# Kernel tuning notes

Hardware: AMD Instinct MI355X
Metric: run time of the kernel (lower is better)

The kernel has to match this reference:

```python
import jax, jax.numpy as jnp
import numpy as np

N = 50000          # nodes
E = 800000         # edges per graph view
D_IN = 256
D_HID = 128
N_CLS = 40
EPS = 1e-12


def agnn_conv(x, src, dst, beta):
    """DGL AGNNConv: cosine edge attention + edge softmax + weighted aggregation."""
    # L2-normalize node features (F.normalize, eps=1e-12)
    norm = jnp.sqrt(jnp.sum(x * x, axis=1, keepdims=True))
    hn = x / jnp.maximum(norm, EPS)                      # [N, D]
    # cosine similarity per edge, scaled by learned beta
    e = beta * jnp.sum(hn[src] * hn[dst], axis=1)        # [E]
    # segment (per-destination) stable softmax
    m = jax.ops.segment_max(e, dst, num_segments=N)      # [N]
    m = jnp.where(jnp.isfinite(m), m, 0.0)               # empty segments -> -inf
    ee = jnp.exp(e - m[dst])                             # [E]
    s = jax.ops.segment_sum(ee, dst, num_segments=N)     # [N]
    a = ee / jnp.maximum(s[dst], EPS)                    # [E]
    # weighted sparse aggregation of ORIGINAL (un-normalized) features
    return jax.ops.segment_sum(a[:, None] * x[src], dst, num_segments=N)


def setup_inputs() -> dict:
    key = jax.random.key(0)
    ks = jax.random.split(key, 10)
    return {
        "input_features": jax.random.normal(ks[0], (N, D_IN), dtype=jnp.float32),
        "src1": jax.random.randint(ks[1], (E,), 0, N, dtype=jnp.int32),
        "dst1": jax.random.randint(ks[2], (E,), 0, N, dtype=jnp.int32),
        "src2": jax.random.randint(ks[3], (E,), 0, N, dtype=jnp.int32),
        "dst2": jax.random.randint(ks[4], (E,), 0, N, dtype=jnp.int32),
        "order_attn": jax.random.uniform(ks[5], (2,), dtype=jnp.float32),
        "W1": jax.random.normal(ks[6], (D_IN, D_HID), dtype=jnp.float32) * (2.0 / np.sqrt(D_IN + D_HID)),
        "b1": jnp.zeros((D_HID,), dtype=jnp.float32),
        "W2": jax.random.normal(ks[7], (D_HID, N_CLS), dtype=jnp.float32) * (2.0 / np.sqrt(D_HID + N_CLS)),
        "b2": jnp.zeros((N_CLS,), dtype=jnp.float32),
        "beta1": jnp.ones((), dtype=jnp.float32),
        "beta2": jnp.ones((), dtype=jnp.float32),
    }


def reference(input_features, src1, dst1, src2, dst2, order_attn, W1, b1, W2, b2, beta1, beta2):
    # fc1 + relu
    x1 = jax.nn.relu(input_features @ W1 + b1)           # [N, D_HID]
    # layer1 over both graph views, combined by learned order_attn scalars
    x2 = order_attn[0] * agnn_conv(x1, src1, dst1, beta1) \
       + order_attn[1] * agnn_conv(x1, src2, dst2, beta1)
    # layer2 over both views
    x3 = order_attn[0] * agnn_conv(x2, src1, dst1, beta2) \
       + order_attn[1] * agnn_conv(x2, src2, dst2, beta2)
    # fc2 (original computes F.log_softmax but discards it; returns logits)
    return x3 @ W2 + b2                                   # [N, N_CLS]
```

## Files before the change

### kernel.cpp

```cpp
#include <hip/hip_runtime.h>
#include <hip/hip_fp16.h>
#include <math.h>

#define NNODES 50000
#define NEDGES 800000
#define DIN    256
#define DHID   128
#define NCLS   40

#define BW    128
#define NBK   391
#define CAP   6144
#define PPART 128
#define CHUNK 6250

typedef _Float16 h2v __attribute__((ext_vector_type(2)));
union HF8 { float4 f; __half2 h2[4]; h2v v[4]; };
union HF4 { float2 f; __half2 h2[2]; };

__global__ __launch_bounds__(256) void fc1_kernel(
    const float* __restrict__ X, const float* __restrict__ W1,
    const float* __restrict__ b1, __half* __restrict__ x1h,
    float* __restrict__ inv1)
{
  __shared__ float As[64][65];
  __shared__ float Bs[64][132];
  const int tid   = threadIdx.x;
  const int node0 = blockIdx.x * 64;
  const int tx    = tid & 15;
  const int ty    = tid >> 4;

  const int ml   = tid >> 2;
  const int kq   = tid & 3;
  const int mrow = (node0 + ml < NNODES) ? node0 + ml : NNODES - 1;

  float acc[4][8];
#pragma unroll
  for (int i = 0; i < 4; ++i)
#pragma unroll
    for (int j = 0; j < 8; ++j) acc[i][j] = 0.f;

  for (int kt = 0; kt < 4; ++kt) {
    const int k0 = kt * 64;
#pragma unroll
    for (int q = 0; q < 4; ++q) {
      const int kk = kq * 16 + q * 4;
      const float4 v = *(const float4*)(X + (size_t)mrow * DIN + k0 + kk);
      As[kk + 0][ml] = v.x; As[kk + 1][ml] = v.y;
      As[kk + 2][ml] = v.z; As[kk + 3][ml] = v.w;
    }
#pragma unroll
    for (int q = 0; q < 8; ++q) {
      const int flat = q * 1024 + tid * 4;
      const int kk = flat >> 7, nn = flat & 127;
      *(float4*)&Bs[kk][nn] = *(const float4*)(W1 + (size_t)(k0 + kk) * DHID + nn);
    }
    __syncthreads();

#pragma unroll 4
    for (int k = 0; k < 64; ++k) {
      const float4 a  = *(const float4*)&As[k][ty * 4];
      const float4 b0 = *(const float4*)&Bs[k][tx * 4];
      const float4 b1v= *(const float4*)&Bs[k][64 + tx * 4];
      const float av[4] = {a.x, a.y, a.z, a.w};
      const float bv[8] = {b0.x, b0.y, b0.z, b0.w, b1v.x, b1v.y, b1v.z, b1v.w};
#pragma unroll
      for (int i = 0; i < 4; ++i)
#pragma unroll
        for (int j = 0; j < 8; ++j) acc[i][j] += av[i] * bv[j];
    }
    __syncthreads();
  }

  const float4 bb0 = *(const float4*)(b1 + tx * 4);
  const float4 bb1 = *(const float4*)(b1 + 64 + tx * 4);
  const float bias[8] = {bb0.x, bb0.y, bb0.z, bb0.w, bb1.x, bb1.y, bb1.z, bb1.w};

#pragma unroll
  for (int i = 0; i < 4; ++i) {
    const int row = node0 + ty * 4 + i;
    float v[8];
    float q = 0.f;
#pragma unroll
    for (int j = 0; j < 8; ++j) {
      float t = acc[i][j] + bias[j];
      t = t > 0.f ? t : 0.f;
      v[j] = t;
      q += t * t;
    }
    q += __shfl_xor(q, 1);
    q += __shfl_xor(q, 2);
    q += __shfl_xor(q, 4);
    q += __shfl_xor(q, 8);
    if (row < NNODES) {
      HF4 o0, o1;
      o0.h2[0] = __floats2half2_rn(v[0], v[1]);
      o0.h2[1] = __floats2half2_rn(v[2], v[3]);
      o1.h2[0] = __floats2half2_rn(v[4], v[5]);
      o1.h2[1] = __floats2half2_rn(v[6], v[7]);
      *(float2*)(x1h + (size_t)row * DHID + tx * 4)      = o0.f;
      *(float2*)(x1h + (size_t)row * DHID + 64 + tx * 4) = o1.f;
      if (tx == 0) inv1[row] = 1.0f / fmaxf(sqrtf(q), 1e-12f);
    }
  }
}

__global__ __launch_bounds__(320) void fc2_kernel(
    const float* __restrict__ x3, const float* __restrict__ W2,
    const float* __restrict__ b2, float* __restrict__ out)
{
  __shared__ float Xs[8][DHID];
  const int tid   = threadIdx.x;
  const int node0 = blockIdx.x * 8;
  for (int idx = tid; idx < 8 * DHID; idx += 320)
    Xs[idx >> 7][idx & 127] = x3[(size_t)node0 * DHID + idx];
  __syncthreads();

  const int ns = tid / NCLS;
  const int c  = tid - ns * NCLS;
  float acc = b2[c];
#pragma unroll 8
  for (int k = 0; k < DHID; ++k) acc += Xs[ns][k] * W2[k * NCLS + c];
  out[(size_t)(node0 + ns) * NCLS + c] = acc;
}

__global__ __launch_bounds__(256) void hist_part_kernel(
    const int* __restrict__ dst1, const int* __restrict__ dst2,
    int* __restrict__ H)
{
  const int bid = blockIdx.x;
  const int v   = bid >= PPART;
  const int p   = v ? bid - PPART : bid;
  const int* __restrict__ dst = v ? dst2 : dst1;

  __shared__ int hist[NBK];
  for (int i = threadIdx.x; i < NBK; i += 256) hist[i] = 0;
  __syncthreads();
  const int beg = p * CHUNK;
  const int end = (beg + CHUNK < NEDGES) ? beg + CHUNK : NEDGES;
  for (int j = beg + threadIdx.x; j < end; j += 256)
    atomicAdd(&hist[dst[j] >> 7], 1);
  __syncthreads();
  for (int i = threadIdx.x; i < NBK; i += 256)
    H[(v * NBK + i) * PPART + p] = hist[i];
}

__global__ __launch_bounds__(128) void scan_bucket_kernel(
    int* __restrict__ H, int* __restrict__ btot)
{
  const int b   = blockIdx.x;
  const int tid = threadIdx.x;
  __shared__ int sm[PPART];
  const int v = H[b * PPART + tid];
  sm[tid] = v;
  __syncthreads();
  for (int off = 1; off < PPART; off <<= 1) {
    int t = (tid >= off) ? sm[tid - off] : 0;
    __syncthreads();
    sm[tid] += t;
    __syncthreads();
  }
  H[b * PPART + tid] = sm[tid] - v;
  if (tid == PPART - 1) btot[b] = sm[tid];
}

__global__ __launch_bounds__(1024) void scan_btot_kernel(
    const int* __restrict__ btot, int* __restrict__ boffG)
{
  __shared__ int sm[1024];
  const int tid = threadIdx.x;
  const int v = (tid < 2 * NBK) ? btot[tid] : 0;
  sm[tid] = v;
  __syncthreads();
  for (int off = 1; off < 1024; off <<= 1) {
    int t = (tid >= off) ? sm[tid - off] : 0;
    __syncthreads();
    sm[tid] += t;
    __syncthreads();
  }
  if (tid < 2 * NBK) boffG[tid] = sm[tid] - v;
  if (tid == 0) boffG[2 * NBK] = 2 * NEDGES;
}

__global__ __launch_bounds__(256) void scatter_part_kernel(
    const int* __restrict__ src1, const int* __restrict__ dst1,
    const int* __restrict__ src2, const int* __restrict__ dst2,
    const int* __restrict__ H, const int* __restrict__ boffG,
    int2* __restrict__ st)
{
  const int bid = blockIdx.x;
  const int v   = bid >= PPART;
  const int p   = v ? bid - PPART : bid;
  const int* __restrict__ src = v ? src2 : src1;
  const int* __restrict__ dst = v ? dst2 : dst1;

  __shared__ int lcur[NBK];
  for (int i = threadIdx.x; i < NBK; i += 256)
    lcur[i] = boffG[v * NBK + i] + H[(v * NBK + i) * PPART + p];
  __syncthreads();
  const int beg = p * CHUNK;
  const int end = (beg + CHUNK < NEDGES) ? beg + CHUNK : NEDGES;
  for (int j = beg + threadIdx.x; j < end; j += 256) {
    const int s = src[j], d = dst[j];
    const int k = atomicAdd(&lcur[d >> 7], 1);
    st[k] = make_int2(s, d);
  }
}

__global__ __launch_bounds__(256) void build_buckets_kernel(
    const int2* __restrict__ st, const int* __restrict__ boffG,
    int* __restrict__ rp1, int* __restrict__ rp2,
    int* __restrict__ col1, int* __restrict__ col2)
{
  const int bid = blockIdx.x;
  const int v   = bid >= NBK;
  const int b   = v ? bid - NBK : bid;
  int* __restrict__ rp  = v ? rp2 : rp1;
  int* __restrict__ col = v ? col2 : col1;
  const int tid = threadIdx.x;

  const int off0G  = boffG[bid];
  const int cnt    = boffG[bid + 1] - off0G;
  const int off0   = off0G - v * NEDGES;
  const int base_d = b * BW;
  const int nd     = (NNODES - base_d < BW) ? (NNODES - base_d) : BW;

  __shared__ int deg[BW];
  __shared__ int loff[BW + 1];
  __shared__ int cur[BW];
  __shared__ int lcol[CAP];

  if (tid < BW) deg[tid] = 0;
  __syncthreads();
  for (int j = tid; j < cnt; j += 256)
    atomicAdd(&deg[st[off0G + j].y - base_d], 1);
  __syncthreads();

  if (tid == 0) loff[0] = 0;
  if (tid < BW) loff[tid + 1] = deg[tid];
  __syncthreads();
  for (int off = 1; off < BW; off <<= 1) {
    int t = (tid < BW && tid + 1 >= off) ? loff[tid + 1 - off] : 0;
    __syncthreads();
    if (tid < BW && tid + 1 >= off) loff[tid + 1] += t;
    __syncthreads();
  }
  if (tid < nd) rp[base_d + tid] = off0 + loff[tid];
  if (tid == 0 && b == NBK - 1) rp[NNODES] = NEDGES;
  if (tid < BW) cur[tid] = loff[tid];
  __syncthreads();

  if (cnt <= CAP) {
    for (int j = tid; j < cnt; j += 256) {
      const int2 pr = st[off0G + j];
      const int k = atomicAdd(&cur[pr.y - base_d], 1);
      lcol[k] = pr.x;
    }
    __syncthreads();
    if (tid < nd) {
      const int s0 = loff[tid], s1 = s0 + deg[tid];
      for (int a = s0 + 1; a < s1; ++a) {
        const int key = lcol[a];
        int c = a - 1;
        while (c >= s0 && lcol[c] > key) { lcol[c + 1] = lcol[c]; --c; }
        lcol[c + 1] = key;
      }
    }
    __syncthreads();
    for (int j = tid; j < cnt; j += 256) col[off0 + j] = lcol[j];
  } else {
    for (int j = tid; j < cnt; j += 256) {
      const int2 pr = st[off0G + j];
      const int k = atomicAdd(&cur[pr.y - base_d], 1);
      col[off0 + k] = pr.x;
    }
    __syncthreads();
    if (tid < nd) {
      const int s0 = off0 + loff[tid], s1 = s0 + deg[tid];
      for (int a = s0 + 1; a < s1; ++a) {
        const int key = col[a];
        int c = a - 1;
        while (c >= s0 && col[c] > key) { col[c + 1] = col[c]; --c; }
        col[c + 1] = key;
      }
    }
  }
}

__global__ __launch_bounds__(256) void agnn_layer_kernel(
    const __half* __restrict__ xh, const float* __restrict__ inv,
    const int* __restrict__ rp1, const int* __restrict__ col1,
    const int* __restrict__ rp2, const int* __restrict__ col2,
    const float* __restrict__ beta_p, const float* __restrict__ order_attn,
    __half* __restrict__ yh_out, float* __restrict__ inv_out,
    float* __restrict__ y32_out, int n)
{
  const int wid  = (blockIdx.x * blockDim.x + threadIdx.x) >> 6;
  if (wid >= n) return;
  const int lane = threadIdx.x & 63;
  const int grp  = lane >> 4;
  const int sub  = lane & 15;

  const float beta = beta_p[0];
  const float bi   = beta * inv[wid];

  HF8 ud; ud.f = *(const float4*)(xh + (size_t)wid * DHID + sub * 8);

  const int beg1 = rp1[wid], end1 = rp1[wid + 1];
  const int beg2 = rp2[wid], end2 = rp2[wid + 1];

  float s1 = 0.f, s2 = 0.f;
  float y1[8], y2[8];
#pragma unroll
  for (int k = 0; k < 8; ++k) { y1[k] = 0.f; y2[k] = 0.f; }

  int j1 = beg1 + grp, j2 = beg2 + grp;
  int sa1 = col1[j1 < end1 ? j1 : 0];
  int sa2 = col2[j2 < end2 ? j2 : 0];

  while (j1 < end1 || j2 < end2) {
    const bool p1 = j1 < end1;
    const bool p2 = j2 < end2;
    const int  c1 = sa1, c2 = sa2;

    const float isa1 = inv[c1];
    const float isa2 = inv[c2];
    HF8 u1; u1.f = *(const float4*)(xh + (size_t)c1 * DHID + sub * 8);
    HF8 u2; u2.f = *(const float4*)(xh + (size_t)c2 * DHID + sub * 8);

    const int nj1 = j1 + 4, nj2 = j2 + 4;
    sa1 = col1[nj1 < end1 ? nj1 : 0];
    sa2 = col2[nj2 < end2 ? nj2 : 0];

    float d1 = 0.f, d2 = 0.f;
#pragma unroll
    for (int i = 0; i < 4; ++i) {
      d1 = __builtin_amdgcn_fdot2(u1.v[i], ud.v[i], d1, false);
      d2 = __builtin_amdgcn_fdot2(u2.v[i], ud.v[i], d2, false);
    }
#pragma unroll
    for (int off = 1; off <= 8; off <<= 1) {
      d1 += __shfl_xor(d1, off);
      d2 += __shfl_xor(d2, off);
    }

    const float w1 = p1 ? __expf(bi * isa1 * d1) : 0.f;
    const float w2 = p2 ? __expf(bi * isa2 * d2) : 0.f;
    s1 += w1; s2 += w2;
#pragma unroll
    for (int i = 0; i < 4; ++i) {
      y1[2 * i + 0] = fmaf(w1, (float)u1.v[i][0], y1[2 * i + 0]);
      y1[2 * i + 1] = fmaf(w1, (float)u1.v[i][1], y1[2 * i + 1]);
      y2[2 * i + 0] = fmaf(w2, (float)u2.v[i][0], y2[2 * i + 0]);
      y2[2 * i + 1] = fmaf(w2, (float)u2.v[i][1], y2[2 * i + 1]);
    }

    j1 = nj1; j2 = nj2;
  }

  s1 += __shfl_xor(s1, 16); s1 += __shfl_xor(s1, 32);
  s2 += __shfl_xor(s2, 16); s2 += __shfl_xor(s2, 32);
#pragma unroll
  for (int k = 0; k < 8; ++k) {
    y1[k] += __shfl_xor(y1[k], 16); y1[k] += __shfl_xor(y1[k], 32);
    y2[k] += __shfl_xor(y2[k], 16); y2[k] += __shfl_xor(y2[k], 32);
  }

  const float r1 = (end1 > beg1) ? order_attn[0] / fmaxf(s1, 1e-12f) : 0.f;
  const float r2 = (end2 > beg2) ? order_attn[1] / fmaxf(s2, 1e-12f) : 0.f;
  float acc[8];
#pragma unroll
  for (int k = 0; k < 8; ++k) acc[k] = r1 * y1[k] + r2 * y2[k];

  if (inv_out) {
    float ss = 0.f;
#pragma unroll
    for (int k = 0; k < 8; ++k) ss += acc[k] * acc[k];
    ss += __shfl_xor(ss, 1);
    ss += __shfl_xor(ss, 2);
    ss += __shfl_xor(ss, 4);
    ss += __shfl_xor(ss, 8);
    if (lane == 0) inv_out[wid] = 1.0f / fmaxf(sqrtf(ss), 1e-12f);
  }

  if (grp == 0) {
    if (yh_out) {
      HF8 o;
      o.h2[0] = __floats2half2_rn(acc[0], acc[1]);
      o.h2[1] = __floats2half2_rn(acc[2], acc[3]);
      o.h2[2] = __floats2half2_rn(acc[4], acc[5]);
      o.h2[3] = __floats2half2_rn(acc[6], acc[7]);
      *(float4*)(yh_out + (size_t)wid * DHID + sub * 8) = o.f;
    }
    if (y32_out) {
      float* yp = y32_out + (size_t)wid * DHID + sub * 8;
      *(float4*)(yp)     = make_float4(acc[0], acc[1], acc[2], acc[3]);
      *(float4*)(yp + 4) = make_float4(acc[4], acc[5], acc[6], acc[7]);
    }
  }
}

extern "C" void kernel_launch(void* const* d_in, const int* in_sizes, int n_in,
                              void* d_out, int out_size, void* d_ws, size_t ws_size,
                              hipStream_t stream)
{
  const float* X          = (const float*)d_in[0];
  const int*   src1       = (const int*)d_in[1];
  const int*   dst1       = (const int*)d_in[2];
  const int*   src2       = (const int*)d_in[3];
  const int*   dst2       = (const int*)d_in[4];
  const float* order_attn = (const float*)d_in[5];
  const float* W1         = (const float*)d_in[6];
  const float* b1         = (const float*)d_in[7];
  const float* W2         = (const float*)d_in[8];
  const float* b2         = (const float*)d_in[9];
  const float* beta1      = (const float*)d_in[10];
  const float* beta2      = (const float*)d_in[11];
  float*       out        = (float*)d_out;

  char*  ws  = (char*)d_ws;
  size_t off = 0;
  auto alloc = [&](size_t bytes) -> void* {
    void* p = ws + off;
    off += (bytes + 255) & ~size_t(255);
    return p;
  };
  __half* x1h  = (__half*)alloc((size_t)NNODES * DHID * 2);
  __half* x2h  = (__half*)alloc((size_t)NNODES * DHID * 2);
  float*  x3   = (float*)alloc((size_t)NNODES * DHID * 4);
  float*  inv1 = (float*)alloc((size_t)NNODES * 4);
  float*  inv2 = (float*)alloc((size_t)NNODES * 4);
  int*    rp1  = (int*)alloc((size_t)(NNODES + 1) * 4);
  int*    rp2  = (int*)alloc((size_t)(NNODES + 1) * 4);
  int*    col1 = (int*)alloc((size_t)NEDGES * 4);
  int*    col2 = (int*)alloc((size_t)NEDGES * 4);
  int*    H    = (int*)alloc((size_t)2 * NBK * PPART * 4);
  int*    btot = (int*)alloc((size_t)2 * NBK * 4);
  int*    boffG= (int*)alloc((size_t)(2 * NBK + 1) * 4);
  int2*   st   = (int2*)x3;

  const int WB = (NNODES + 3) / 4;

  hist_part_kernel<<<2 * PPART, 256, 0, stream>>>(dst1, dst2, H);
  scan_bucket_kernel<<<2 * NBK, 128, 0, stream>>>(H, btot);
  scan_btot_kernel<<<1, 1024, 0, stream>>>(btot, boffG);
  scatter_part_kernel<<<2 * PPART, 256, 0, stream>>>(src1, dst1, src2, dst2,
                                                     H, boffG, st);
  build_buckets_kernel<<<2 * NBK, 256, 0, stream>>>(st, boffG, rp1, rp2, col1, col2);

  fc1_kernel<<<(NNODES + 63) / 64, 256, 0, stream>>>(X, W1, b1, x1h, inv1);

  agnn_layer_kernel<<<WB, 256, 0, stream>>>(x1h, inv1, rp1, col1, rp2, col2,
                                            beta1, order_attn,
                                            x2h, inv2, nullptr, NNODES);
  agnn_layer_kernel<<<WB, 256, 0, stream>>>(x2h, inv2, rp1, col1, rp2, col2,
                                            beta2, order_attn,
                                            nullptr, nullptr, x3, NNODES);

  fc2_kernel<<<NNODES / 8, 320, 0, stream>>>(x3, W2, b2, out);
}
```

Before: 300.4 us.

## Use DPP row reductions, fp16 final layer output, padded column arrays, 32-bit indexing

Replaces the shuffle-based 16-lane reductions with DPP row operations. It stores the second AGNN layer output in fp16 instead of fp32, which halves the write and the fc2 read. The column index arrays are padded with zeros so the prefetch loads need no bounds select, and 32-bit unsigned address arithmetic replaces 64-bit. The sort staging buffer now gets its own allocation because x3 shrank, and the fp16 x3 adds some precision loss before fc2.

```diff
diff --git a/kernel.cpp b/kernel.cpp
--- a/kernel.cpp
+++ b/kernel.cpp
@@ -13,10 +13,24 @@
 #define CAP   6144
 #define PPART 128
 #define CHUNK 6250
+#define CPAD  64
 
 typedef _Float16 h2v __attribute__((ext_vector_type(2)));
 union HF8 { float4 f; __half2 h2[4]; h2v v[4]; };
 union HF4 { float2 f; __half2 h2[2]; };
+
+template <int CTRL>
+__device__ __forceinline__ float dpp_add(float d) {
+  int t = __builtin_amdgcn_update_dpp(0, __float_as_int(d), CTRL, 0xf, 0xf, true);
+  return d + __int_as_float(t);
+}
+__device__ __forceinline__ float rowsum16(float d) {
+  d = dpp_add<0xB1>(d);
+  d = dpp_add<0x4E>(d);
+  d = dpp_add<0x141>(d);
+  d = dpp_add<0x128>(d);
+  return d;
+}
 
 __global__ __launch_bounds__(256) void fc1_kernel(
     const float* __restrict__ X, const float* __restrict__ W1,
@@ -88,10 +102,7 @@
       v[j] = t;
       q += t * t;
     }
-    q += __shfl_xor(q, 1);
-    q += __shfl_xor(q, 2);
-    q += __shfl_xor(q, 4);
-    q += __shfl_xor(q, 8);
+    q = rowsum16(q);
     if (row < NNODES) {
       HF4 o0, o1;
       o0.h2[0] = __floats2half2_rn(v[0], v[1]);
@@ -106,14 +117,21 @@
 }
 
 __global__ __launch_bounds__(320) void fc2_kernel(
-    const float* __restrict__ x3, const float* __restrict__ W2,
+    const __half* __restrict__ x3h, const float* __restrict__ W2,
     const float* __restrict__ b2, float* __restrict__ out)
 {
   __shared__ float Xs[8][DHID];
   const int tid   = threadIdx.x;
   const int node0 = blockIdx.x * 8;
-  for (int idx = tid; idx < 8 * DHID; idx += 320)
-    Xs[idx >> 7][idx & 127] = x3[(size_t)node0 * DHID + idx];
+  if (tid < 128) {
+    HF8 u; u.f = *(const float4*)(x3h + (size_t)node0 * DHID + tid * 8);
+    float* dst = &Xs[0][0] + tid * 8;
+#pragma unroll
+    for (int i = 0; i < 4; ++i) {
+      const float2 t = __half22float2(u.h2[i]);
+      dst[2 * i] = t.x; dst[2 * i + 1] = t.y;
+    }
+  }
   __syncthreads();
 
   const int ns = tid / NCLS;
@@ -165,10 +183,13 @@
 }
 
 __global__ __launch_bounds__(1024) void scan_btot_kernel(
-    const int* __restrict__ btot, int* __restrict__ boffG)
+    const int* __restrict__ btot, int* __restrict__ boffG,
+    int* __restrict__ col1, int* __restrict__ col2)
 {
   __shared__ int sm[1024];
   const int tid = threadIdx.x;
+  if (tid >= 768 && tid < 768 + CPAD) col1[NEDGES + tid - 768] = 0;
+  if (tid >= 832 && tid < 832 + CPAD) col2[NEDGES + tid - 832] = 0;
   const int v = (tid < 2 * NBK) ? btot[tid] : 0;
   sm[tid] = v;
   __syncthreads();
@@ -300,11 +321,12 @@
   const int lane = threadIdx.x & 63;
   const int grp  = lane >> 4;
   const int sub  = lane & 15;
+  const unsigned subo = (unsigned)sub * 8u;
 
   const float beta = beta_p[0];
   const float bi   = beta * inv[wid];
 
-  HF8 ud; ud.f = *(const float4*)(xh + (size_t)wid * DHID + sub * 8);
+  HF8 ud; ud.f = *(const float4*)(xh + ((unsigned)wid * 128u + subo));
 
   const int beg1 = rp1[wid], end1 = rp1[wid + 1];
   const int beg2 = rp2[wid], end2 = rp2[wid + 1];
@@ -315,22 +337,21 @@
   for (int k = 0; k < 8; ++k) { y1[k] = 0.f; y2[k] = 0.f; }
 
   int j1 = beg1 + grp, j2 = beg2 + grp;
-  int sa1 = col1[j1 < end1 ? j1 : 0];
-  int sa2 = col2[j2 < end2 ? j2 : 0];
+  int c1 = col1[j1];
+  int c2 = col2[j2];
 
   while (j1 < end1 || j2 < end2) {
     const bool p1 = j1 < end1;
     const bool p2 = j2 < end2;
-    const int  c1 = sa1, c2 = sa2;
-
-    const float isa1 = inv[c1];
-    const float isa2 = inv[c2];
-    HF8 u1; u1.f = *(const float4*)(xh + (size_t)c1 * DHID + sub * 8);
-    HF8 u2; u2.f = *(const float4*)(xh + (size_t)c2 * DHID + sub * 8);
+
+    const float is1 = inv[(unsigned)c1];
+    const float is2 = inv[(unsigned)c2];
+    HF8 u1; u1.f = *(const float4*)(xh + ((unsigned)c1 * 128u + subo));
+    HF8 u2; u2.f = *(const float4*)(xh + ((unsigned)c2 * 128u + subo));
 
     const int nj1 = j1 + 4, nj2 = j2 + 4;
-    sa1 = col1[nj1 < end1 ? nj1 : 0];
-    sa2 = col2[nj2 < end2 ? nj2 : 0];
+    c1 = col1[nj1];
+    c2 = col2[nj2];
 
     float d1 = 0.f, d2 = 0.f;
 #pragma unroll
@@ -338,14 +359,11 @@
       d1 = __builtin_amdgcn_fdot2(u1.v[i], ud.v[i], d1, false);
       d2 = __builtin_amdgcn_fdot2(u2.v[i], ud.v[i], d2, false);
     }
-#pragma unroll
-    for (int off = 1; off <= 8; off <<= 1) {
-      d1 += __shfl_xor(d1, off);
-      d2 += __shfl_xor(d2, off);
-    }
-
-    const float w1 = p1 ? __expf(bi * isa1 * d1) : 0.f;
-    const float w2 = p2 ? __expf(bi * isa2 * d2) : 0.f;
+    d1 = rowsum16(d1);
+    d2 = rowsum16(d2);
+
+    const float w1 = p1 ? __expf(bi * is1 * d1) : 0.f;
+    const float w2 = p2 ? __expf(bi * is2 * d2) : 0.f;
     s1 += w1; s2 += w2;
 #pragma unroll
     for (int i = 0; i < 4; ++i) {
@@ -376,10 +394,7 @@
     float ss = 0.f;
 #pragma unroll
     for (int k = 0; k < 8; ++k) ss += acc[k] * acc[k];
-    ss += __shfl_xor(ss, 1);
-    ss += __shfl_xor(ss, 2);
-    ss += __shfl_xor(ss, 4);
-    ss += __shfl_xor(ss, 8);
+    ss = rowsum16(ss);
     if (lane == 0) inv_out[wid] = 1.0f / fmaxf(sqrtf(ss), 1e-12f);
   }
 
@@ -390,7 +405,7 @@
       o.h2[1] = __floats2half2_rn(acc[2], acc[3]);
       o.h2[2] = __floats2half2_rn(acc[4], acc[5]);
       o.h2[3] = __floats2half2_rn(acc[6], acc[7]);
-      *(float4*)(yh_out + (size_t)wid * DHID + sub * 8) = o.f;
+      *(float4*)(yh_out + ((unsigned)wid * 128u + subo)) = o.f;
     }
     if (y32_out) {
       float* yp = y32_out + (size_t)wid * DHID + sub * 8;
@@ -427,23 +442,23 @@
   };
   __half* x1h  = (__half*)alloc((size_t)NNODES * DHID * 2);
   __half* x2h  = (__half*)alloc((size_t)NNODES * DHID * 2);
-  float*  x3   = (float*)alloc((size_t)NNODES * DHID * 4);
+  __half* x3h  = (__half*)alloc((size_t)NNODES * DHID * 2);
   float*  inv1 = (float*)alloc((size_t)NNODES * 4);
   float*  inv2 = (float*)alloc((size_t)NNODES * 4);
   int*    rp1  = (int*)alloc((size_t)(NNODES + 1) * 4);
   int*    rp2  = (int*)alloc((size_t)(NNODES + 1) * 4);
-  int*    col1 = (int*)alloc((size_t)NEDGES * 4);
-  int*    col2 = (int*)alloc((size_t)NEDGES * 4);
+  int*    col1 = (int*)alloc((size_t)(NEDGES + CPAD) * 4);
+  int*    col2 = (int*)alloc((size_t)(NEDGES + CPAD) * 4);
   int*    H    = (int*)alloc((size_t)2 * NBK * PPART * 4);
   int*    btot = (int*)alloc((size_t)2 * NBK * 4);
   int*    boffG= (int*)alloc((size_t)(2 * NBK + 1) * 4);
-  int2*   st   = (int2*)x3;
+  int2*   st   = (int2*)alloc((size_t)2 * NEDGES * 8);
 
   const int WB = (NNODES + 3) / 4;
 
   hist_part_kernel<<<2 * PPART, 256, 0, stream>>>(dst1, dst2, H);
   scan_bucket_kernel<<<2 * NBK, 128, 0, stream>>>(H, btot);
-  scan_btot_kernel<<<1, 1024, 0, stream>>>(btot, boffG);
+  scan_btot_kernel<<<1, 1024, 0, stream>>>(btot, boffG, col1, col2);
   scatter_part_kernel<<<2 * PPART, 256, 0, stream>>>(src1, dst1, src2, dst2,
                                                      H, boffG, st);
   build_buckets_kernel<<<2 * NBK, 256, 0, stream>>>(st, boffG, rp1, rp2, col1, col2);
@@ -455,7 +470,7 @@
                                             x2h, inv2, nullptr, NNODES);
   agnn_layer_kernel<<<WB, 256, 0, stream>>>(x2h, inv2, rp1, col1, rp2, col2,
                                             beta2, order_attn,
-                                            nullptr, nullptr, x3, NNODES);
-
-  fc2_kernel<<<NNODES / 8, 320, 0, stream>>>(x3, W2, b2, out);
-}
+                                            x3h, nullptr, nullptr, NNODES);
+
+  fc2_kernel<<<NNODES / 8, 320, 0, stream>>>(x3h, W2, b2, out);
+}
```

After: 284.7 us. 1.06x faster.
